# Kernel tuning notes

Hardware: AMD Instinct MI355X
Metric: run time of the kernel (lower is better)

The kernel has to match this reference:

```python
import jax, jax.numpy as jnp
import numpy as np


def setup_inputs() -> dict:
    key = jax.random.key(0)
    k1, k2, k3, k4, k5 = jax.random.split(key, 5)
    B, S, E, H = 1024, 512, 50, 50
    bound = 1.0 / np.sqrt(H)  # PyTorch LSTM init range
    hidden_state = jax.random.normal(k1, (B, S, E), dtype=jnp.float32)
    W_ih = jax.random.uniform(k2, (4 * H, E), dtype=jnp.float32, minval=-bound, maxval=bound)
    W_hh = jax.random.uniform(k3, (4 * H, H), dtype=jnp.float32, minval=-bound, maxval=bound)
    b_ih = jax.random.uniform(k4, (4 * H,), dtype=jnp.float32, minval=-bound, maxval=bound)
    b_hh = jax.random.uniform(k5, (4 * H,), dtype=jnp.float32, minval=-bound, maxval=bound)
    return {"hidden_state": hidden_state, "W_ih": W_ih, "W_hh": W_hh, "b_ih": b_ih, "b_hh": b_hh}


def reference(hidden_state, W_ih, W_hh, b_ih, b_hh):
    # hidden_state: (B, S, E). Single-layer unidirectional LSTM, h0=c0=0.
    B, S, E = hidden_state.shape
    H = W_hh.shape[1]
    # Precompute input-to-gate projections for all timesteps: (S, B, 4H)
    xg = jnp.einsum('bse,ge->sbg', hidden_state, W_ih) + (b_ih + b_hh)

    def step(carry, xt):
        h, c = carry
        gates = xt + h @ W_hh.T  # (B, 4H)
        i, f, g, o = jnp.split(gates, 4, axis=-1)  # PyTorch gate order i,f,g,o
        i = jax.nn.sigmoid(i)
        f = jax.nn.sigmoid(f)
        g = jnp.tanh(g)
        o = jax.nn.sigmoid(o)
        c = f * c + i * g
        h = o * jnp.tanh(c)
        return (h, c), None

    h0 = jnp.zeros((B, H), dtype=hidden_state.dtype)
    c0 = jnp.zeros((B, H), dtype=hidden_state.dtype)
    (h_final, _), _ = jax.lax.scan(step, (h0, c0), xg)
    # PyTorch returns h_n of shape (num_layers, B, H); module transposes to (B, num_layers, H)
    return h_final[:, None, :]
```

## Files before the change

### kernel.cpp

```cpp
#include <hip/hip_runtime.h>


typedef __attribute__((ext_vector_type(8))) _Float16 f16x8;
typedef __attribute__((ext_vector_type(4))) float f32x4;

__device__ __forceinline__ float fast_sigmoid(float z) {
  return __builtin_amdgcn_rcpf(1.0f + __expf(-z));
}
__device__ __forceinline__ float fast_tanh(float z) {
  return 1.0f - 2.0f * __builtin_amdgcn_rcpf(1.0f + __expf(2.0f * z));
}

__global__ __launch_bounds__(512, 1) void lstm_fused(
    const float* __restrict__ xg,
    const float* __restrict__ W_ih,
    const float* __restrict__ W_hh,
    const float* __restrict__ b_ih,
    const float* __restrict__ b_hh,
    float* __restrict__ out)
{
  constexpr int S = 512, E = 50, H = 50;
  const int tid  = threadIdx.x;
  const int lane = tid & 63;
  const int wv   = tid >> 6;
  const int c0   = blockIdx.x << 2;

  __shared__ __align__(16) unsigned char lds[3072];
  for (int i = tid; i < 3072 / 4; i += 512) reinterpret_cast<unsigned*>(lds)[i] = 0u;

  const int m  = lane & 15;
  const int kg = lane >> 4;
  const int tstart = 2 * wv;
  const int ntiles = (wv < 6) ? 2 : ((wv == 6) ? 1 : 0);

  f16x8 wfr[2][4];
  f32x4 bias[2];
#pragma unroll
  for (int i = 0; i < 2; ++i) {
    const int  mt    = tstart + i;
    const bool tv    = (i < ntiles);
    const int  j     = mt * 16 + m;
    const int  hh    = j >> 2, g = j & 3;
    const bool rowok = tv && (hh < H);
#pragma unroll
    for (int kt = 0; kt < 4; ++kt) {
      f16x8 s;
#pragma unroll
      for (int jj = 0; jj < 8; ++jj) {
        const int k = kt * 32 + kg * 8 + jj;
        float w = 0.0f;
        if (rowok) {
          if (k < 50)                  w = W_ih[(g * 50 + hh) * 50 + k];
          else if (k >= 64 && k < 114) w = W_hh[(g * 50 + hh) * 50 + (k - 64)];
        }
        s[jj] = (_Float16)w;
      }
      wfr[i][kt] = s;
    }
    f32x4 bv;
#pragma unroll
    for (int r = 0; r < 4; ++r) {
      const int jr = mt * 16 + kg * 4 + r;
      const int hr = jr >> 2, gr = jr & 3;
      bv[r] = (tv && hr < H) ? (b_ih[gr * 50 + hr] + b_hh[gr * 50 + hr]) : 0.0f;
    }
    bias[i] = bv;
  }

  float cst = 0.0f;

  const bool isstg = (wv == 7);
  bool     sok[4];
  long     gb[4];
  unsigned la[4];
  float    A[4], B[4];
#pragma unroll
  for (int u = 0; u < 4; ++u) {
    const int xs = lane + 64 * u;
    sok[u] = isstg && (xs < 200);
    const int chn = sok[u] ? (xs / 50) : 0;
    const int e   = sok[u] ? (xs - 50 * chn) : 0;
    gb[u] = ((long)(c0 + chn) * S) * E + e;
    la[u] = (unsigned)(((e >> 5) << 8) + (chn << 6) + ((e & 31) << 1));
    A[u] = 0.f; B[u] = 0.f;
  }

  __syncthreads();

#pragma unroll
  for (int u = 0; u < 4; ++u) {
    if (sok[u]) {
      *reinterpret_cast<_Float16*>(lds + 0 * 512 + la[u]) = (_Float16)xg[gb[u] + 0 * E];
      *reinterpret_cast<_Float16*>(lds + 1 * 512 + la[u]) = (_Float16)xg[gb[u] + 1 * E];
    }
  }
#pragma unroll
  for (int u = 0; u < 4; ++u) {
    if (sok[u]) { A[u] = xg[gb[u] + 2 * E]; B[u] = xg[gb[u] + 3 * E]; }
  }
  __syncthreads();

  const unsigned bro = (unsigned)(((lane & 3) << 6) + (kg << 4));

  f16x8 b2{}, b3{}, nb0{}, nb1{};

  f32x4 xcur[2];
  {
    if (m < 4) {
      nb0 = *reinterpret_cast<const f16x8*>(lds + 0u + bro);
      nb1 = *reinterpret_cast<const f16x8*>(lds + 256u + bro);
    }
#pragma unroll
    for (int i = 0; i < 2; ++i) {
      f32x4 a = bias[i];
      a = __builtin_amdgcn_mfma_f32_16x16x32_f16(wfr[i][0], nb0, a, 0, 0, 0);
      a = __builtin_amdgcn_mfma_f32_16x16x32_f16(wfr[i][1], nb1, a, 0, 0, 0);
      xcur[i] = a;
    }
  }

  auto step = [&](int t, float (&P)[4]) {
    if (ntiles > 0) {
      const unsigned hs = 2048u + (unsigned)(t & 1) * 512u;
      const unsigned xs = (unsigned)((t + 1) & 3) * 512u;
      if (m < 4) {
        b2  = *reinterpret_cast<const f16x8*>(lds + hs + bro);
        b3  = *reinterpret_cast<const f16x8*>(lds + hs + 256u + bro);
        nb0 = *reinterpret_cast<const f16x8*>(lds + xs + bro);
        nb1 = *reinterpret_cast<const f16x8*>(lds + xs + 256u + bro);
      }

      f32x4 acc0 = xcur[0];
      acc0 = __builtin_amdgcn_mfma_f32_16x16x32_f16(wfr[0][2], b2, acc0, 0, 0, 0);
      acc0 = __builtin_amdgcn_mfma_f32_16x16x32_f16(wfr[0][3], b3, acc0, 0, 0, 0);
      f32x4 acc1 = xcur[1];
      acc1 = __builtin_amdgcn_mfma_f32_16x16x32_f16(wfr[1][2], b2, acc1, 0, 0, 0);
      acc1 = __builtin_amdgcn_mfma_f32_16x16x32_f16(wfr[1][3], b3, acc1, 0, 0, 0);

      float gv[4];
#pragma unroll
      for (int r = 0; r < 4; ++r) {
        const int sp = __builtin_amdgcn_update_dpp(
            0, __float_as_int(acc1[r]), 0x114 , 0xF, 0xF, true);
        gv[r] = (m < 4) ? acc0[r] : __int_as_float(sp);
      }

      const int ti = m >> 2;
      const int h  = 4 * (tstart + ti) + kg;
      if ((m < 8) && (ti < ntiles) && (h < H)) {
        const float ig = fast_sigmoid(gv[0]);
        const float fg = fast_sigmoid(gv[1]);
        const float gg = fast_tanh   (gv[2]);
        const float og = fast_sigmoid(gv[3]);
        const float c  = fg * cst + ig * gg;
        cst = c;
        const float hv = og * fast_tanh(c);
        const int ch = m & 3;
        if (t == S - 1) {
          out[(long)(c0 + ch) * H + h] = hv;
        } else {
          *reinterpret_cast<_Float16*>(
              lds + 2048u + (unsigned)((t + 1) & 1) * 512u +
              (unsigned)(((h >> 5) << 8) + (ch << 6) + ((h & 31) << 1))) = (_Float16)hv;
        }
      }

      {
        f32x4 c0v = bias[0];
        c0v = __builtin_amdgcn_mfma_f32_16x16x32_f16(wfr[0][0], nb0, c0v, 0, 0, 0);
        c0v = __builtin_amdgcn_mfma_f32_16x16x32_f16(wfr[0][1], nb1, c0v, 0, 0, 0);
        xcur[0] = c0v;
        f32x4 c1v = bias[1];
        c1v = __builtin_amdgcn_mfma_f32_16x16x32_f16(wfr[1][0], nb0, c1v, 0, 0, 0);
        c1v = __builtin_amdgcn_mfma_f32_16x16x32_f16(wfr[1][1], nb1, c1v, 0, 0, 0);
        xcur[1] = c1v;
      }
    } else if (isstg) {
      if (t + 2 < S) {
        const unsigned sl = (unsigned)((t + 2) & 3) * 512u;
#pragma unroll
        for (int u = 0; u < 4; ++u)
          if (sok[u]) *reinterpret_cast<_Float16*>(lds + sl + la[u]) = (_Float16)P[u];
        if (t + 4 < S) {
#pragma unroll
          for (int u = 0; u < 4; ++u)
            if (sok[u]) P[u] = xg[gb[u] + (long)(t + 4) * E];
        }
      }
    }
    __syncthreads();
  };

  for (int t = 0; t < S; t += 2) {
    step(t, A);
    step(t + 1, B);
  }
}

extern "C" void kernel_launch(void* const* d_in, const int* in_sizes, int n_in,
                              void* d_out, int out_size, void* d_ws, size_t ws_size,
                              hipStream_t stream) {
  const float* x    = (const float*)d_in[0];
  const float* W_ih = (const float*)d_in[1];
  const float* W_hh = (const float*)d_in[2];
  const float* b_ih = (const float*)d_in[3];
  const float* b_hh = (const float*)d_in[4];
  float* out = (float*)d_out;
  hipLaunchKernelGGL(lstm_fused, dim3(256), dim3(512), 0, stream,
                     x, W_ih, W_hh, b_ih, b_hh, out);
}
```

Measured before the change: 200.4 us.

## Batch input projections for three timesteps per MFMA pass and redistribute via DPP

Instead of computing the input-to-gate MFMA for the next timestep every step, each wave now computes x-projections for three future timesteps at once, using different 4-column groups of the B operand, then scatters results to per-step registers with DPP row shifts. The staging wave keeps a deeper 4-slot LDS ring with loads issued further ahead. The goal is to cut the per-step MFMA count on the serial critical path. It adds DPP shuffles and more register pressure, and the loop unroll by six with a tail must line up exactly with the ring indexing.

```diff
diff --git a/kernel.cpp b/kernel.cpp
--- a/kernel.cpp
+++ b/kernel.cpp
@@ -33,7 +33,7 @@
   const int tstart = 2 * wv;
   const int ntiles = (wv < 6) ? 2 : ((wv == 6) ? 1 : 0);
 
-  f16x8 wfr[2][4];
+  f16x8 wxf[2][2], whf[2][2];
   f32x4 bias[2];
 #pragma unroll
   for (int i = 0; i < 2; ++i) {
@@ -55,7 +55,7 @@
         }
         s[jj] = (_Float16)w;
       }
-      wfr[i][kt] = s;
+      if (kt < 2) wxf[i][kt] = s; else whf[i][kt - 2] = s;
     }
     f32x4 bv;
 #pragma unroll
@@ -70,10 +70,8 @@
   float cst = 0.0f;
 
   const bool isstg = (wv == 7);
-  bool     sok[4];
-  long     gb[4];
-  unsigned la[4];
-  float    A[4], B[4];
+  bool sok[4]; long gb[4]; unsigned la[4];
+  float R0[4], R1[4];
 #pragma unroll
   for (int u = 0; u < 4; ++u) {
     const int xs = lane + 64 * u;
@@ -82,7 +80,7 @@
     const int e   = sok[u] ? (xs - 50 * chn) : 0;
     gb[u] = ((long)(c0 + chn) * S) * E + e;
     la[u] = (unsigned)(((e >> 5) << 8) + (chn << 6) + ((e & 31) << 1));
-    A[u] = 0.f; B[u] = 0.f;
+    R0[u] = 0.f; R1[u] = 0.f;
   }
 
   __syncthreads();
@@ -90,73 +88,82 @@
 #pragma unroll
   for (int u = 0; u < 4; ++u) {
     if (sok[u]) {
-      *reinterpret_cast<_Float16*>(lds + 0 * 512 + la[u]) = (_Float16)xg[gb[u] + 0 * E];
-      *reinterpret_cast<_Float16*>(lds + 1 * 512 + la[u]) = (_Float16)xg[gb[u] + 1 * E];
+#pragma unroll
+      for (int sl = 0; sl < 4; ++sl)
+        *reinterpret_cast<_Float16*>(lds + sl * 512 + la[u]) = (_Float16)xg[gb[u] + sl * E];
     }
   }
 #pragma unroll
   for (int u = 0; u < 4; ++u) {
-    if (sok[u]) { A[u] = xg[gb[u] + 2 * E]; B[u] = xg[gb[u] + 3 * E]; }
+    if (sok[u]) { R0[u] = xg[gb[u] + 4 * E]; R1[u] = xg[gb[u] + 5 * E]; }
   }
   __syncthreads();
 
   const unsigned bro = (unsigned)(((lane & 3) << 6) + (kg << 4));
-
-  f16x8 b2{}, b3{}, nb0{}, nb1{};
-
-  f32x4 xcur[2];
-  {
-    if (m < 4) {
-      nb0 = *reinterpret_cast<const f16x8*>(lds + 0u + bro);
-      nb1 = *reinterpret_cast<const f16x8*>(lds + 256u + bro);
-    }
-#pragma unroll
-    for (int i = 0; i < 2; ++i) {
-      f32x4 a = bias[i];
-      a = __builtin_amdgcn_mfma_f32_16x16x32_f16(wfr[i][0], nb0, a, 0, 0, 0);
-      a = __builtin_amdgcn_mfma_f32_16x16x32_f16(wfr[i][1], nb1, a, 0, 0, 0);
-      xcur[i] = a;
-    }
-  }
-
-  auto step = [&](int t, float (&P)[4]) {
+  f16x8 b2{}, b3{};
+
+  f32x4 xcA[2], xcB[2], xcC[2];
+
+  auto batch = [&](int t) {
+    const int g  = m >> 2;
+    const int gg = g ? g : 1;
+    const unsigned xa = (unsigned)(((t + gg) & 3) * 512 + ((m & 3) << 6) + (kg << 4));
+    const f16x8 nbA = *reinterpret_cast<const f16x8*>(lds + xa);
+    const f16x8 nbB = *reinterpret_cast<const f16x8*>(lds + xa + 256u);
+    f32x4 x0 = bias[0];
+    x0 = __builtin_amdgcn_mfma_f32_16x16x32_f16(wxf[0][0], nbA, x0, 0, 0, 0);
+    x0 = __builtin_amdgcn_mfma_f32_16x16x32_f16(wxf[0][1], nbB, x0, 0, 0, 0);
+    f32x4 x1 = bias[1];
+    x1 = __builtin_amdgcn_mfma_f32_16x16x32_f16(wxf[1][0], nbA, x1, 0, 0, 0);
+    x1 = __builtin_amdgcn_mfma_f32_16x16x32_f16(wxf[1][1], nbB, x1, 0, 0, 0);
+#pragma unroll
+    for (int r = 0; r < 4; ++r) {
+      xcA[0][r] = __int_as_float(__builtin_amdgcn_update_dpp(0, __float_as_int(x0[r]), 0x104, 0xF, 0xF, true));
+      xcA[1][r] = __int_as_float(__builtin_amdgcn_update_dpp(0, __float_as_int(x1[r]), 0x104, 0xF, 0xF, true));
+      xcB[0][r] = __int_as_float(__builtin_amdgcn_update_dpp(0, __float_as_int(x0[r]), 0x108, 0xF, 0xF, true));
+      xcB[1][r] = __int_as_float(__builtin_amdgcn_update_dpp(0, __float_as_int(x1[r]), 0x108, 0xF, 0xF, true));
+      xcC[0][r] = __int_as_float(__builtin_amdgcn_update_dpp(0, __float_as_int(x0[r]), 0x10C, 0xF, 0xF, true));
+      xcC[1][r] = __int_as_float(__builtin_amdgcn_update_dpp(0, __float_as_int(x1[r]), 0x10C, 0xF, 0xF, true));
+    }
+  };
+
+  if (ntiles > 0) batch(-1);
+  __syncthreads();
+
+  auto step = [&](int t, f32x4 (&xc)[2], float (&SR)[4], bool dobatch, bool last) {
     if (ntiles > 0) {
       const unsigned hs = 2048u + (unsigned)(t & 1) * 512u;
-      const unsigned xs = (unsigned)((t + 1) & 3) * 512u;
       if (m < 4) {
-        b2  = *reinterpret_cast<const f16x8*>(lds + hs + bro);
-        b3  = *reinterpret_cast<const f16x8*>(lds + hs + 256u + bro);
-        nb0 = *reinterpret_cast<const f16x8*>(lds + xs + bro);
-        nb1 = *reinterpret_cast<const f16x8*>(lds + xs + 256u + bro);
-      }
-
-      f32x4 acc0 = xcur[0];
-      acc0 = __builtin_amdgcn_mfma_f32_16x16x32_f16(wfr[0][2], b2, acc0, 0, 0, 0);
-      acc0 = __builtin_amdgcn_mfma_f32_16x16x32_f16(wfr[0][3], b3, acc0, 0, 0, 0);
-      f32x4 acc1 = xcur[1];
-      acc1 = __builtin_amdgcn_mfma_f32_16x16x32_f16(wfr[1][2], b2, acc1, 0, 0, 0);
-      acc1 = __builtin_amdgcn_mfma_f32_16x16x32_f16(wfr[1][3], b3, acc1, 0, 0, 0);
+        b2 = *reinterpret_cast<const f16x8*>(lds + hs + bro);
+        b3 = *reinterpret_cast<const f16x8*>(lds + hs + 256u + bro);
+      }
+      f32x4 acc0 = xc[0];
+      acc0 = __builtin_amdgcn_mfma_f32_16x16x32_f16(whf[0][0], b2, acc0, 0, 0, 0);
+      acc0 = __builtin_amdgcn_mfma_f32_16x16x32_f16(whf[0][1], b3, acc0, 0, 0, 0);
+      f32x4 acc1 = xc[1];
+      acc1 = __builtin_amdgcn_mfma_f32_16x16x32_f16(whf[1][0], b2, acc1, 0, 0, 0);
+      acc1 = __builtin_amdgcn_mfma_f32_16x16x32_f16(whf[1][1], b3, acc1, 0, 0, 0);
+
+      if (dobatch) batch(t);
 
       float gv[4];
 #pragma unroll
       for (int r = 0; r < 4; ++r) {
-        const int sp = __builtin_amdgcn_update_dpp(
-            0, __float_as_int(acc1[r]), 0x114 , 0xF, 0xF, true);
+        const int sp = __builtin_amdgcn_update_dpp(0, __float_as_int(acc1[r]), 0x114, 0xF, 0xF, true);
         gv[r] = (m < 4) ? acc0[r] : __int_as_float(sp);
       }
-
       const int ti = m >> 2;
       const int h  = 4 * (tstart + ti) + kg;
       if ((m < 8) && (ti < ntiles) && (h < H)) {
         const float ig = fast_sigmoid(gv[0]);
         const float fg = fast_sigmoid(gv[1]);
-        const float gg = fast_tanh   (gv[2]);
+        const float gg2 = fast_tanh  (gv[2]);
         const float og = fast_sigmoid(gv[3]);
-        const float c  = fg * cst + ig * gg;
+        const float c  = fg * cst + ig * gg2;
         cst = c;
         const float hv = og * fast_tanh(c);
         const int ch = m & 3;
-        if (t == S - 1) {
+        if (last) {
           out[(long)(c0 + ch) * H + h] = hv;
         } else {
           *reinterpret_cast<_Float16*>(
@@ -164,37 +171,32 @@
               (unsigned)(((h >> 5) << 8) + (ch << 6) + ((h & 31) << 1))) = (_Float16)hv;
         }
       }
-
-      {
-        f32x4 c0v = bias[0];
-        c0v = __builtin_amdgcn_mfma_f32_16x16x32_f16(wfr[0][0], nb0, c0v, 0, 0, 0);
-        c0v = __builtin_amdgcn_mfma_f32_16x16x32_f16(wfr[0][1], nb1, c0v, 0, 0, 0);
-        xcur[0] = c0v;
-        f32x4 c1v = bias[1];
-        c1v = __builtin_amdgcn_mfma_f32_16x16x32_f16(wfr[1][0], nb0, c1v, 0, 0, 0);
-        c1v = __builtin_amdgcn_mfma_f32_16x16x32_f16(wfr[1][1], nb1, c1v, 0, 0, 0);
-        xcur[1] = c1v;
-      }
     } else if (isstg) {
-      if (t + 2 < S) {
-        const unsigned sl = (unsigned)((t + 2) & 3) * 512u;
+      if (t + 4 < S) {
+        const unsigned sl = (unsigned)(t & 3) * 512u;
 #pragma unroll
         for (int u = 0; u < 4; ++u)
-          if (sok[u]) *reinterpret_cast<_Float16*>(lds + sl + la[u]) = (_Float16)P[u];
-        if (t + 4 < S) {
-#pragma unroll
-          for (int u = 0; u < 4; ++u)
-            if (sok[u]) P[u] = xg[gb[u] + (long)(t + 4) * E];
-        }
+          if (sok[u]) *reinterpret_cast<_Float16*>(lds + sl + la[u]) = (_Float16)SR[u];
+      }
+      if (t + 6 < S) {
+#pragma unroll
+        for (int u = 0; u < 4; ++u)
+          if (sok[u]) SR[u] = xg[gb[u] + (long)(t + 6) * E];
       }
     }
     __syncthreads();
   };
 
-  for (int t = 0; t < S; t += 2) {
-    step(t, A);
-    step(t + 1, B);
-  }
+  for (int t0 = 0; t0 + 5 < S; t0 += 6) {
+    step(t0 + 0, xcA, R0, false, false);
+    step(t0 + 1, xcB, R1, false, false);
+    step(t0 + 2, xcC, R0, true,  false);
+    step(t0 + 3, xcA, R1, false, false);
+    step(t0 + 4, xcB, R0, false, false);
+    step(t0 + 5, xcC, R1, true,  false);
+  }
+  step(S - 2, xcA, R0, false, false);
+  step(S - 1, xcB, R1, false, true);
 }
 
 extern "C" void kernel_launch(void* const* d_in, const int* in_sizes, int n_in,
```

Result: no change. 201.8 us (+0.7%).
